# Performance work log

Measured on AMD Instinct MI355X. Metric: run time of the kernel, lower is better.

The kernel has to match this reference:

```python
import jax, jax.numpy as jnp
import numpy as np

G, N, F_IN, H, C = 128, 512, 128, 128, 10
LAMB = 1.0
NEG_SLOPE = 0.2
P_EDGE = 32.0 / N  # avg degree ~32


def setup_inputs() -> dict:
    key = jax.random.key(0)
    ks = jax.random.split(key, 12)
    x = jax.random.normal(ks[0], (G, N, F_IN), dtype=jnp.float32)
    # symmetric 0/1 adjacency without self loops (per-graph dense block)
    a = (jax.random.uniform(ks[1], (G, N, N)) < P_EDGE).astype(jnp.float32)
    adj = jnp.maximum(a, jnp.swapaxes(a, 1, 2)) * (1.0 - jnp.eye(N, dtype=jnp.float32))

    def lin(k, fi, fo):
        return (jax.random.normal(k, (fi, fo), dtype=jnp.float32) / np.float32(np.sqrt(fi)))

    return {
        "x": x, "adj": adj,
        "W1": lin(ks[2], F_IN, H), "b1": jnp.zeros((H,), jnp.float32),
        "W2": lin(ks[3], H, H), "b2": jnp.zeros((H,), jnp.float32),
        "W3": lin(ks[4], H, H), "b3": jnp.zeros((H,), jnp.float32),
        "att1_s": 0.1 * jax.random.normal(ks[5], (H,), dtype=jnp.float32),
        "att1_d": 0.1 * jax.random.normal(ks[6], (H,), dtype=jnp.float32),
        "att2_s": 0.1 * jax.random.normal(ks[7], (H,), dtype=jnp.float32),
        "att2_d": 0.1 * jax.random.normal(ks[8], (H,), dtype=jnp.float32),
        "Wl1": lin(ks[9], 2 * H, H), "bl1": jnp.zeros((H,), jnp.float32),
        "Wl2": lin(ks[10], H, H // 2), "bl2": jnp.zeros((H // 2,), jnp.float32),
        "Wl3": lin(ks[11], H // 2, C), "bl3": jnp.zeros((C,), jnp.float32),
    }


def gcn(x, adj, W, b):
    # GCNConv: D^{-1/2} (A + I) D^{-1/2} X W + b  (self-loop weight 1, edge weights in adj)
    deg = adj.sum(-1) + 1.0                              # [G, n]
    dinv = jax.lax.rsqrt(deg)
    xw = x @ W                                           # [G, n, H]
    agg = jnp.einsum('gij,gjf->gif', adj, dinv[..., None] * xw)
    return dinv[..., None] * agg + (dinv * dinv)[..., None] * xw + b


def info_score(x, adj):
    # HGP-SL node information score: row-wise L1 norm of (I - D^{-1} A) X
    deg = jnp.maximum(adj.sum(-1), 1.0)
    agg = jnp.einsum('gij,gjf->gif', adj, x) / deg[..., None]
    return jnp.sum(jnp.abs(x - agg), axis=-1)            # [G, n]


def hgpsl_pool(x, adj, att_s, att_d, k):
    # top-k node selection by information score, then structure learning:
    # dense (sample=False) path: e_ij = leaky_relu(att.[x_i||x_j]) + lamb*A_ij, softmax over j
    s = info_score(x, adj)
    _, idx = jax.lax.top_k(s, k)                         # [G, k]
    xk = jnp.take_along_axis(x, idx[..., None], axis=1)  # [G, k, H]
    g = jnp.arange(x.shape[0])[:, None, None]
    ak = adj[g, idx[:, :, None], idx[:, None, :]]        # induced adjacency [G, k, k]
    e = jax.nn.leaky_relu((xk @ att_s)[:, :, None] + (xk @ att_d)[:, None, :], NEG_SLOPE)
    attn = jax.nn.softmax(e + LAMB * ak, axis=-1)        # new learned edge weights
    return xk, attn


def readout(x):
    # gmp || gap over nodes
    return jnp.concatenate([x.max(axis=1), x.mean(axis=1)], axis=-1)


def reference(x, adj, W1, b1, W2, b2, W3, b3, att1_s, att1_d, att2_s, att2_d,
              Wl1, bl1, Wl2, bl2, Wl3, bl3):
    h = jax.nn.relu(gcn(x, adj, W1, b1))
    h, a1 = hgpsl_pool(h, adj, att1_s, att1_d, N // 2)
    x1 = readout(h)
    h = jax.nn.relu(gcn(h, a1, W2, b2))
    h, a2 = hgpsl_pool(h, a1, att2_s, att2_d, N // 4)
    x2 = readout(h)
    h = jax.nn.relu(gcn(h, a2, W3, b3))
    x3 = readout(h)
    z = jax.nn.relu(x1) + jax.nn.relu(x2) + jax.nn.relu(x3)
    z = jax.nn.relu(z @ Wl1 + bl1)
    z = jax.nn.relu(z @ Wl2 + bl2)
    return jax.nn.softmax(z @ Wl3 + bl3, axis=-1)
```

## Files before the change

kernel.cpp:

```cpp
#include <hip/hip_runtime.h>

#define Gg   128
#define N1   512
#define FH   128
#define K1   256
#define K2   128

typedef __bf16 bf16x8 __attribute__((ext_vector_type(8)));
typedef float  floatx4 __attribute__((ext_vector_type(4)));

__device__ inline float wredsum(float v) {
#pragma unroll
    for (int o = 32; o; o >>= 1) v += __shfl_xor(v, o, 64);
    return v;
}
__device__ inline float wredmax(float v) {
#pragma unroll
    for (int o = 32; o; o >>= 1) v = fmaxf(v, __shfl_xor(v, o, 64));
    return v;
}
__device__ inline unsigned short bf_rne(float x) {
    unsigned u = __float_as_uint(x);
    return (unsigned short)((u + 0x7fffu + ((u >> 16) & 1u)) >> 16);
}
__device__ __forceinline__ void gll16(const void* gsrc, void* lds) {
    __builtin_amdgcn_global_load_lds(
        (const __attribute__((address_space(1))) unsigned int*)gsrc,
        (__attribute__((address_space(3))) unsigned int*)lds, 16, 0, 0);
}

__global__ __launch_bounds__(256) void k_prep_gemm(const float* __restrict__ adj,
        unsigned short* __restrict__ adjbf,
        float* __restrict__ dinv_gcn, float* __restrict__ dinv_info,
        const float* __restrict__ A, const float* __restrict__ W, float* __restrict__ C) {
    __shared__ float Al[64][36];
    __shared__ float Wl[32][132];
    if (blockIdx.x < Gg * N1 / 64) {
        long long row0 = (long long)blockIdx.x * 64;
        int tid = threadIdx.x, tr = tid >> 4, tc = tid & 15;
        float acc[4][8] = {};
        for (int ch = 0; ch < 4; ++ch) {
            for (int p = tid; p < 512; p += 256) {
                int r = p >> 3, c4 = p & 7;
                *(float4*)&Al[r][c4 * 4] = *(const float4*)(A + (row0 + r) * 128 + ch * 32 + c4 * 4);
            }
            for (int p = tid; p < 1024; p += 256) {
                int r = p >> 5, c4 = p & 31;
                *(float4*)&Wl[r][c4 * 4] = *(const float4*)(W + (ch * 32 + r) * 128 + c4 * 4);
            }
            __syncthreads();
            for (int k = 0; k < 32; ++k) {
                float4 w0 = *(const float4*)&Wl[k][tc * 8];
                float4 w1 = *(const float4*)&Wl[k][tc * 8 + 4];
                float w[8] = {w0.x, w0.y, w0.z, w0.w, w1.x, w1.y, w1.z, w1.w};
#pragma unroll
                for (int i = 0; i < 4; ++i) {
                    float a = Al[tr * 4 + i][k];
#pragma unroll
                    for (int j = 0; j < 8; ++j) acc[i][j] = fmaf(a, w[j], acc[i][j]);
                }
            }
            __syncthreads();
        }
#pragma unroll
        for (int i = 0; i < 4; ++i) {
            long long r = row0 + tr * 4 + i;
            *(float4*)(C + r * 128 + tc * 8)     = make_float4(acc[i][0], acc[i][1], acc[i][2], acc[i][3]);
            *(float4*)(C + r * 128 + tc * 8 + 4) = make_float4(acc[i][4], acc[i][5], acc[i][6], acc[i][7]);
        }
    } else {
        int wave = threadIdx.x >> 6, lane = threadIdx.x & 63;
        long long row = (long long)(blockIdx.x - Gg * N1 / 64) * 4 + wave;
        const float* ar = adj + row * N1;
        float s = 0.f;
        unsigned short ub[8] __attribute__((aligned(16)));
#pragma unroll
        for (int c = 0; c < 2; ++c) {
            float4 v = *(const float4*)(ar + lane * 8 + c * 4);
            s += (v.x + v.y) + (v.z + v.w);
            ub[c * 4 + 0] = (unsigned short)(__float_as_uint(v.x) >> 16);
            ub[c * 4 + 1] = (unsigned short)(__float_as_uint(v.y) >> 16);
            ub[c * 4 + 2] = (unsigned short)(__float_as_uint(v.z) >> 16);
            ub[c * 4 + 3] = (unsigned short)(__float_as_uint(v.w) >> 16);
        }
        *(uint4*)(adjbf + row * N1 + lane * 8) = *(const uint4*)ub;
        s = wredsum(s);
        if (lane == 0) {
            dinv_gcn[row]  = rsqrtf(s + 1.0f);
            dinv_info[row] = 1.0f / fmaxf(s, 1.0f);
        }
    }
}

__global__ __launch_bounds__(256) void k_tsplit(const float* __restrict__ feat,
        const float* __restrict__ rs,
        unsigned short* __restrict__ Thi, unsigned short* __restrict__ Tmid,
        unsigned short* __restrict__ Tlo) {
    __shared__ float tile[64 * 65];
    int b = blockIdx.x;
    int g = b >> 4, rb = (b >> 1) & 7, cb = b & 1;
    int t = threadIdx.x;
    {
        int r0 = t >> 4, c4 = t & 15;
#pragma unroll
        for (int i = 0; i < 4; ++i) {
            int r = r0 + i * 16;
            float4 v = *(const float4*)(feat + ((long long)g * 512 + rb * 64 + r) * 128 + cb * 64 + c4 * 4);
            if (rs) {
                float sc = rs[(long long)g * 512 + rb * 64 + r];
                v.x *= sc; v.y *= sc; v.z *= sc; v.w *= sc;
            }
            tile[r * 65 + c4 * 4 + 0] = v.x;
            tile[r * 65 + c4 * 4 + 1] = v.y;
            tile[r * 65 + c4 * 4 + 2] = v.z;
            tile[r * 65 + c4 * 4 + 3] = v.w;
        }
    }
    __syncthreads();
    int tf = t >> 2, chunk = t & 3;
    unsigned short hbuf[16] __attribute__((aligned(16)));
    unsigned short mbuf[16] __attribute__((aligned(16)));
    unsigned short lbuf[16] __attribute__((aligned(16)));
#pragma unroll
    for (int i = 0; i < 16; ++i) {
        int m = chunk * 16 + i;
        float v = tile[m * 65 + tf];
        unsigned short h = bf_rne(v);
        float fh = __uint_as_float((unsigned)h << 16);
        float r1 = v - fh;
        unsigned short md = bf_rne(r1);
        float fm = __uint_as_float((unsigned)md << 16);
        float r2 = r1 - fm;
        unsigned short lo = bf_rne(r2);
        hbuf[i] = h; mbuf[i] = md; lbuf[i] = lo;
    }
    int sxz = (tf >> 1) & 3;
    int c0 = (chunk & 1) * 2;
    int p0 = (c0 ^ sxz) * 8, p1 = ((c0 + 1) ^ sxz) * 8;
    long long obase = (long long)g * 65536 + (rb * 2 + (chunk >> 1)) * 4096
                    + (cb * 64 + tf) * 32;
    *(uint4*)(Thi + obase + p0)  = *(const uint4*)&hbuf[0];
    *(uint4*)(Thi + obase + p1)  = *(const uint4*)&hbuf[8];
    *(uint4*)(Tmid + obase + p0) = *(const uint4*)&mbuf[0];
    *(uint4*)(Tmid + obase + p1) = *(const uint4*)&mbuf[8];
    *(uint4*)(Tlo + obase + p0)  = *(const uint4*)&lbuf[0];
    *(uint4*)(Tlo + obase + p1)  = *(const uint4*)&lbuf[8];
}

template<int EPI>
__global__ __launch_bounds__(256) void k_aggmm(const unsigned short* __restrict__ adjbf,
        const unsigned short* __restrict__ Bhi, const unsigned short* __restrict__ Bmid,
        const unsigned short* __restrict__ Blo,
        const float* __restrict__ dvec, const float* __restrict__ hx,
        const float* __restrict__ bias, float* __restrict__ outH, float* __restrict__ outS) {
    __shared__ unsigned short Al[2][4096];
    __shared__ unsigned short Blin[2][3][4096];
    __shared__ float sred[2][128];
    int b = blockIdx.x;
    int g  = (b & 7) + ((b >> 5) << 3);
    int rb = (b >> 3) & 3;
    int tid = threadIdx.x;
    int w = tid >> 6, lane = tid & 63;
    int wm = w >> 1, wn = w & 1;
    int ln = lane & 15, quad = lane >> 4;
    int aoff = ((quad ^ ((lane >> 1) & 3)) << 4);
    floatx4 acc[4][4];
#pragma unroll
    for (int i = 0; i < 4; ++i)
#pragma unroll
        for (int j = 0; j < 4; ++j) { floatx4 z = {0.f, 0.f, 0.f, 0.f}; acc[i][j] = z; }

    const char* bsrc0 = (const char*)(Bhi  + (long long)g * 65536);
    const char* bsrc1 = (const char*)(Bmid + (long long)g * 65536);
    const char* bsrc2 = (const char*)(Blo  + (long long)g * 65536);
    int r1 = w * 32 + (lane >> 2);
    int c1 = (lane & 3) ^ ((r1 >> 1) & 3);
    int r2 = r1 + 16;
    int c2 = (lane & 3) ^ ((r2 >> 1) & 3);
    const unsigned short* abase = adjbf + ((long long)g * 512 + rb * 128) * 512;
    const unsigned short* asrc1 = abase + (long long)r1 * 512 + c1 * 8;
    const unsigned short* asrc2 = abase + (long long)r2 * 512 + c2 * 8;

#define STAGE(bi, kkv) do {                                                   \
        char* aldst = (char*)&Al[bi][0] + w * 2048;                           \
        gll16(asrc1 + (kkv), aldst);                                          \
        gll16(asrc2 + (kkv), aldst + 1024);                                   \
        long long soff = (long long)((kkv) >> 5) * 8192 + (w * 2048) + (lane << 4); \
        char* l0 = (char*)&Blin[bi][0][0] + w * 2048;                         \
        char* l1 = (char*)&Blin[bi][1][0] + w * 2048;                         \
        char* l2 = (char*)&Blin[bi][2][0] + w * 2048;                         \
        gll16(bsrc0 + soff,        l0);                                       \
        gll16(bsrc0 + soff + 1024, l0 + 1024);                                \
        gll16(bsrc1 + soff,        l1);                                       \
        gll16(bsrc1 + soff + 1024, l1 + 1024);                                \
        gll16(bsrc2 + soff,        l2);                                       \
        gll16(bsrc2 + soff + 1024, l2 + 1024);                                \
    } while (0)

    STAGE(0, 0);
    for (int kk = 0; kk < 512; kk += 32) {
        int cur = (kk >> 5) & 1;
        if (kk + 32 < 512) {
            STAGE(cur ^ 1, kk + 32);
            asm volatile("s_waitcnt vmcnt(8)" ::: "memory");
        } else {
            asm volatile("s_waitcnt vmcnt(0)" ::: "memory");
        }
        __builtin_amdgcn_sched_barrier(0);
        __builtin_amdgcn_s_barrier();
        bf16x8 af[4];
#pragma unroll
        for (int tm = 0; tm < 4; ++tm)
            af[tm] = *(const bf16x8*)((const char*)&Al[cur][0] + (wm * 64 + tm * 16 + ln) * 64 + aoff);
#pragma unroll
        for (int s = 0; s < 3; ++s) {
#pragma unroll
            for (int tn = 0; tn < 4; ++tn) {
                bf16x8 bfr = *(const bf16x8*)((const char*)&Blin[cur][s][0]
                                              + (wn * 64 + tn * 16 + ln) * 64 + aoff);
#pragma unroll
                for (int tm = 0; tm < 4; ++tm)
                    acc[tm][tn] = __builtin_amdgcn_mfma_f32_16x16x32_bf16(af[tm], bfr, acc[tm][tn], 0, 0, 0);
            }
        }
        __builtin_amdgcn_sched_barrier(0);
        __builtin_amdgcn_s_barrier();
    }
#undef STAGE
    long long rowbase = (long long)g * 512 + rb * 128;
    if (EPI == 0) {
#pragma unroll
        for (int tm = 0; tm < 4; ++tm)
#pragma unroll
        for (int r = 0; r < 4; ++r) {
            int ml = wm * 64 + tm * 16 + quad * 4 + r;
            long long grow = rowbase + ml;
            float di = dvec[grow];
#pragma unroll
            for (int tn = 0; tn < 4; ++tn) {
                int nc = wn * 64 + tn * 16 + ln;
                float hv = hx[grow * 128 + nc];
                float o = fmaxf(fmaf(di, acc[tm][tn][r] + di * hv, bias[nc]), 0.f);
                outH[grow * 128 + nc] = o;
            }
        }
    } else {
#pragma unroll
        for (int tm = 0; tm < 4; ++tm)
#pragma unroll
        for (int r = 0; r < 4; ++r) {
            int ml = wm * 64 + tm * 16 + quad * 4 + r;
            long long grow = rowbase + ml;
            float di = dvec[grow];
            float v = 0.f;
#pragma unroll
            for (int tn = 0; tn < 4; ++tn) {
                int nc = wn * 64 + tn * 16 + ln;
                float hv = hx[grow * 128 + nc];
                v += fabsf(hv - acc[tm][tn][r] * di);
            }
            v += __shfl_xor(v, 1); v += __shfl_xor(v, 2);
            v += __shfl_xor(v, 4); v += __shfl_xor(v, 8);
            if (ln == 0) sred[wn][ml] = v;
        }
        __syncthreads();
        if (tid < 128) outS[rowbase + tid] = sred[0][tid] + sred[1][tid];
    }
}

__global__ __launch_bounds__(256) void k_gemm_rw(const float* __restrict__ A,
        const float* __restrict__ W, float* __restrict__ C,
        const float* __restrict__ rs) {
    __shared__ float Al[64][36];
    __shared__ float Wl[32][132];
    long long row0 = (long long)blockIdx.x * 64;
    int tid = threadIdx.x, tr = tid >> 4, tc = tid & 15;
    float acc[4][8] = {};
    for (int ch = 0; ch < 4; ++ch) {
        for (int p = tid; p < 512; p += 256) {
            int r = p >> 3, c4 = p & 7;
            *(float4*)&Al[r][c4 * 4] = *(const float4*)(A + (row0 + r) * 128 + ch * 32 + c4 * 4);
        }
        for (int p = tid; p < 1024; p += 256) {
            int r = p >> 5, c4 = p & 31;
            *(float4*)&Wl[r][c4 * 4] = *(const float4*)(W + (ch * 32 + r) * 128 + c4 * 4);
        }
        __syncthreads();
        for (int k = 0; k < 32; ++k) {
            float4 w0 = *(const float4*)&Wl[k][tc * 8];
            float4 w1 = *(const float4*)&Wl[k][tc * 8 + 4];
            float w[8] = {w0.x, w0.y, w0.z, w0.w, w1.x, w1.y, w1.z, w1.w};
#pragma unroll
            for (int i = 0; i < 4; ++i) {
                float a = Al[tr * 4 + i][k];
#pragma unroll
                for (int j = 0; j < 8; ++j) acc[i][j] = fmaf(a, w[j], acc[i][j]);
            }
        }
        __syncthreads();
    }
#pragma unroll
    for (int i = 0; i < 4; ++i) {
        long long r = row0 + tr * 4 + i;
        float sc = rs ? rs[r] : 1.0f;
        *(float4*)(C + r * 128 + tc * 8)     = make_float4(sc * acc[i][0], sc * acc[i][1], sc * acc[i][2], sc * acc[i][3]);
        *(float4*)(C + r * 128 + tc * 8 + 4) = make_float4(sc * acc[i][4], sc * acc[i][5], sc * acc[i][6], sc * acc[i][7]);
    }
}

template<int NT, int KSEL>
__global__ __launch_bounds__(256) void k_topk(const float* __restrict__ s, int* __restrict__ idx) {
    __shared__ unsigned long long keys[NT];
    int g = blockIdx.x;
    const float* sg = s + g * NT;
    for (int t = threadIdx.x; t < NT; t += 256) {
        unsigned int b = __float_as_uint(sg[t]);
        unsigned int ord = (b & 0x80000000u) ? ~b : (b | 0x80000000u);
        keys[t] = ((unsigned long long)(~ord) << 32) | (unsigned int)t;
    }
    __syncthreads();
    for (int k = 2; k <= NT; k <<= 1) {
        for (int j = k >> 1; j > 0; j >>= 1) {
            for (int i = threadIdx.x; i < NT; i += 256) {
                int l = i ^ j;
                if (l > i) {
                    bool dir = ((i & k) == 0);
                    unsigned long long a = keys[i], b2 = keys[l];
                    bool sw = dir ? (a > b2) : (a < b2);
                    if (sw) { keys[i] = b2; keys[l] = a; }
                }
            }
            __syncthreads();
        }
    }
    for (int t = threadIdx.x; t < KSEL; t += 256)
        idx[g * KSEL + t] = (int)(keys[t] & 0xffffffffu);
}

template<int KK>
__global__ __launch_bounds__(256) void k_gather(const float* __restrict__ h, int srcN,
        const int* __restrict__ idx, const float* __restrict__ atts, const float* __restrict__ attd,
        float* __restrict__ xk, float* __restrict__ as_, float* __restrict__ ad_) {
    int wave = threadIdx.x >> 6, lane = threadIdx.x & 63;
    int r = blockIdx.x * 4 + wave;
    int g = r / KK;
    int j = idx[r];
    float2 v = *(const float2*)(h + ((long long)g * srcN + j) * 128 + lane * 2);
    *(float2*)(xk + (long long)r * 128 + lane * 2) = v;
    float2 sv = *(const float2*)(atts + lane * 2);
    float2 dv = *(const float2*)(attd + lane * 2);
    float ps = v.x * sv.x + v.y * sv.y;
    float pd = v.x * dv.x + v.y * dv.y;
    ps = wredsum(ps); pd = wredsum(pd);
    if (lane == 0) { as_[r] = ps; ad_[r] = pd; }
}

template<int KK, int SRCN, bool BF16>
__global__ __launch_bounds__(256) void k_attnro(const void* __restrict__ adjSrc,
        const int* __restrict__ idx, const float* __restrict__ as_, const float* __restrict__ ad_,
        float* __restrict__ attn, float* __restrict__ dgo, float* __restrict__ dio,
        const float* __restrict__ xk, float* __restrict__ xo) {
    constexpr int E = KK / 64;
    constexpr int nAttn = Gg * KK / 4;
    __shared__ int   idxL[KK];
    __shared__ float adL[KK];
    __shared__ float rowL[4][SRCN];
    if ((int)blockIdx.x >= nAttn) {
        int g = blockIdx.x - nAttn, t = threadIdx.x;
        if (t < 128) {
            const float* p = xk + (long long)g * KK * 128 + t;
            float m = -1e30f, s = 0.f;
            for (int r = 0; r < KK; ++r) { float v = p[r * 128]; m = fmaxf(m, v); s += v; }
            xo[g * 256 + t] = m;
            xo[g * 256 + 128 + t] = s * (1.0f / KK);
        }
        return;
    }
    int bpg = KK / 4;
    int g = blockIdx.x / bpg;
    int wave = threadIdx.x >> 6, lane = threadIdx.x & 63;
    int i = (blockIdx.x % bpg) * 4 + wave;
    for (int t = threadIdx.x; t < KK; t += 256) { idxL[t] = idx[g * KK + t]; adL[t] = ad_[g * KK + t]; }
    __syncthreads();
    int ri = idxL[i];
    if (BF16) {
        const unsigned short* arow = (const unsigned short*)adjSrc + ((long long)g * SRCN + ri) * SRCN;
        for (int c = lane; c < SRCN; c += 64)
            rowL[wave][c] = __uint_as_float((unsigned)arow[c] << 16);
    } else {
        const float* arow = (const float*)adjSrc + ((long long)g * SRCN + ri) * SRCN;
        for (int c = lane; c < SRCN; c += 64) rowL[wave][c] = arow[c];
    }
    float asi = as_[g * KK + i];
    float vals[E];
    float m = -1e30f;
#pragma unroll
    for (int e = 0; e < E; ++e) {
        int j = e * 64 + lane;
        float x = asi + adL[j];
        x = (x >= 0.f) ? x : 0.2f * x;
        x += rowL[wave][idxL[j]];
        vals[e] = x; m = fmaxf(m, x);
    }
    m = wredmax(m);
    float S = 0.f;
#pragma unroll
    for (int e = 0; e < E; ++e) { vals[e] = expf(vals[e] - m); S += vals[e]; }
    S = wredsum(S);
    float inv = 1.f / S, rs = 0.f;
    float* orow = attn + ((long long)g * KK + i) * KK;
#pragma unroll
    for (int e = 0; e < E; ++e) { float p = vals[e] * inv; rs += p; orow[e * 64 + lane] = p; }
    rs = wredsum(rs);
    if (lane == 0) { dgo[g * KK + i] = rsqrtf(rs + 1.f); dio[g * KK + i] = 1.f / fmaxf(rs, 1.f); }
}

template<int KK, bool SCALEY, int EPI>
__global__ __launch_bounds__(256) void k_agg(const float* __restrict__ A, const float* __restrict__ Y,
        const float* __restrict__ dg, const float* __restrict__ di_,
        const float* __restrict__ bias, const float* __restrict__ hx,
        float* __restrict__ outH, float* __restrict__ outS) {
    __shared__ float Al[64][36];
    __shared__ float Yl[32][132];
    constexpr int RB = KK / 64;
    int g = blockIdx.x / RB;
    int rb = blockIdx.x % RB;
    const float* Ag = A + (long long)g * KK * KK;
    const float* Yg = Y + (long long)g * KK * 128;
    int tid = threadIdx.x, tr = tid >> 4, tc = tid & 15;
    float acc[4][8] = {};
    for (int ch = 0; ch < KK / 32; ++ch) {
        for (int p = tid; p < 512; p += 256) {
            int r = p >> 3, c4 = p & 7;
            *(float4*)&Al[r][c4 * 4] = *(const float4*)(Ag + (long long)(rb * 64 + r) * KK + ch * 32 + c4 * 4);
        }
        for (int p = tid; p < 1024; p += 256) {
            int r = p >> 5, c4 = p & 31;
            float4 v = *(const float4*)(Yg + (ch * 32 + r) * 128 + c4 * 4);
            if (SCALEY) { float sc = dg[g * KK + ch * 32 + r]; v.x *= sc; v.y *= sc; v.z *= sc; v.w *= sc; }
            *(float4*)&Yl[r][c4 * 4] = v;
        }
        __syncthreads();
        for (int k = 0; k < 32; ++k) {
            float4 w0 = *(const float4*)&Yl[k][tc * 8];
            float4 w1 = *(const float4*)&Yl[k][tc * 8 + 4];
            float w[8] = {w0.x, w0.y, w0.z, w0.w, w1.x, w1.y, w1.z, w1.w};
#pragma unroll
            for (int i = 0; i < 4; ++i) {
                float a = Al[tr * 4 + i][k];
#pragma unroll
                for (int j = 0; j < 8; ++j) acc[i][j] = fmaf(a, w[j], acc[i][j]);
            }
        }
        __syncthreads();
    }
    int i0 = rb * 64 + tr * 4;
    if (EPI == 0) {
#pragma unroll
        for (int i = 0; i < 4; ++i) {
            long long gi = (long long)g * KK + i0 + i;
            float d = dg[gi], dd = d * d;
            float4 x0 = *(const float4*)(hx + gi * 128 + tc * 8);
            float4 x1 = *(const float4*)(hx + gi * 128 + tc * 8 + 4);
            float4 b0 = *(const float4*)(bias + tc * 8);
            float4 b1 = *(const float4*)(bias + tc * 8 + 4);
            float4 o0, o1;
            o0.x = fmaxf(fmaf(d, acc[i][0], fmaf(dd, x0.x, b0.x)), 0.f);
            o0.y = fmaxf(fmaf(d, acc[i][1], fmaf(dd, x0.y, b0.y)), 0.f);
            o0.z = fmaxf(fmaf(d, acc[i][2], fmaf(dd, x0.z, b0.z)), 0.f);
            o0.w = fmaxf(fmaf(d, acc[i][3], fmaf(dd, x0.w, b0.w)), 0.f);
            o1.x = fmaxf(fmaf(d, acc[i][4], fmaf(dd, x1.x, b1.x)), 0.f);
            o1.y = fmaxf(fmaf(d, acc[i][5], fmaf(dd, x1.y, b1.y)), 0.f);
            o1.z = fmaxf(fmaf(d, acc[i][6], fmaf(dd, x1.z, b1.z)), 0.f);
            o1.w = fmaxf(fmaf(d, acc[i][7], fmaf(dd, x1.w, b1.w)), 0.f);
            *(float4*)(outH + gi * 128 + tc * 8)     = o0;
            *(float4*)(outH + gi * 128 + tc * 8 + 4) = o1;
        }
    } else {
        float* red = &Al[0][0];
#pragma unroll
        for (int i = 0; i < 4; ++i) {
            long long gi = (long long)g * KK + i0 + i;
            float d = di_[gi];
            float4 x0 = *(const float4*)(hx + gi * 128 + tc * 8);
            float4 x1 = *(const float4*)(hx + gi * 128 + tc * 8 + 4);
            float p = fabsf(x0.x - acc[i][0] * d) + fabsf(x0.y - acc[i][1] * d)
                    + fabsf(x0.z - acc[i][2] * d) + fabsf(x0.w - acc[i][3] * d)
                    + fabsf(x1.x - acc[i][4] * d) + fabsf(x1.y - acc[i][5] * d)
                    + fabsf(x1.z - acc[i][6] * d) + fabsf(x1.w - acc[i][7] * d);
            red[(tr * 4 + i) * 17 + tc] = p;
        }
        __syncthreads();
        if (tid < 64) {
            float s = 0.f;
#pragma unroll
            for (int t = 0; t < 16; ++t) s += red[tid * 17 + t];
            outS[(long long)g * KK + rb * 64 + tid] = s;
        }
    }
}

__global__ __launch_bounds__(128) void k_mlp(const float* __restrict__ x1, const float* __restrict__ x2,
        const float* __restrict__ h3,
        const float* __restrict__ Wl1, const float* __restrict__ bl1,
        const float* __restrict__ Wl2, const float* __restrict__ bl2,
        const float* __restrict__ Wl3, const float* __restrict__ bl3,
        float* __restrict__ out) {
    __shared__ float z[256], z1[128], z2[64], lg[10];
    int g = blockIdx.x, t = threadIdx.x;
    {
        const float* p = h3 + (long long)g * K2 * 128 + t;
        float m = -1e30f, s = 0.f;
        for (int r = 0; r < K2; ++r) { float v = p[r * 128]; m = fmaxf(m, v); s += v; }
        float x3a = m, x3b = s * (1.0f / K2);
        z[t]       = fmaxf(x1[g * 256 + t], 0.f)       + fmaxf(x2[g * 256 + t], 0.f)       + fmaxf(x3a, 0.f);
        z[t + 128] = fmaxf(x1[g * 256 + 128 + t], 0.f) + fmaxf(x2[g * 256 + 128 + t], 0.f) + fmaxf(x3b, 0.f);
    }
    __syncthreads();
    {
        float acc = bl1[t];
        for (int k = 0; k < 256; ++k) acc = fmaf(z[k], Wl1[k * 128 + t], acc);
        z1[t] = fmaxf(acc, 0.f);
    }
    __syncthreads();
    if (t < 64) {
        float acc = bl2[t];
        for (int k = 0; k < 128; ++k) acc = fmaf(z1[k], Wl2[k * 64 + t], acc);
        z2[t] = fmaxf(acc, 0.f);
    }
    __syncthreads();
    if (t < 10) {
        float acc = bl3[t];
        for (int k = 0; k < 64; ++k) acc = fmaf(z2[k], Wl3[k * 10 + t], acc);
        lg[t] = acc;
    }
    __syncthreads();
    if (t == 0) {
        float m = -1e30f;
        for (int c = 0; c < 10; ++c) m = fmaxf(m, lg[c]);
        float S = 0.f;
        float e[10];
        for (int c = 0; c < 10; ++c) { e[c] = expf(lg[c] - m); S += e[c]; }
        float inv = 1.f / S;
        for (int c = 0; c < 10; ++c) out[g * 10 + c] = e[c] * inv;
    }
}

extern "C" void kernel_launch(void* const* d_in, const int* in_sizes, int n_in,
                              void* d_out, int out_size, void* d_ws, size_t ws_size,
                              hipStream_t stream) {
    const float* x     = (const float*)d_in[0];
    const float* adj   = (const float*)d_in[1];
    const float* W1    = (const float*)d_in[2];
    const float* b1    = (const float*)d_in[3];
    const float* W2    = (const float*)d_in[4];
    const float* b2    = (const float*)d_in[5];
    const float* W3    = (const float*)d_in[6];
    const float* b3    = (const float*)d_in[7];
    const float* att1s = (const float*)d_in[8];
    const float* att1d = (const float*)d_in[9];
    const float* att2s = (const float*)d_in[10];
    const float* att2d = (const float*)d_in[11];
    const float* Wl1   = (const float*)d_in[12];
    const float* bl1   = (const float*)d_in[13];
    const float* Wl2   = (const float*)d_in[14];
    const float* bl2   = (const float*)d_in[15];
    const float* Wl3   = (const float*)d_in[16];
    const float* bl3   = (const float*)d_in[17];
    float* out = (float*)d_out;

    char* ws = (char*)d_ws;
    unsigned short* Thi  = (unsigned short*)(ws + 0);
    unsigned short* Tmid = (unsigned short*)(ws + 16777216);
    unsigned short* Tlo  = (unsigned short*)(ws + 33554432);
    float* xk1 = (float*)(ws + 0);
    float* xw2 = (float*)(ws + 16777216);
    float* h2  = (float*)(ws + 33554432);
    float* xk2 = (float*)(ws + 16777216);
    float* a2  = (float*)(ws + 25165824);
    float* xw3 = (float*)(ws + 0);
    float* h3  = (float*)(ws + 8388608);
    float* dxw1 = (float*)(ws + 50331648);
    float* h1   = dxw1;
    float* a1   = dxw1;
    float* s1      = (float*)(ws + 83886080);
    int*   idx1    = (int*)  (ws + 84148224);
    float* as1     = (float*)(ws + 84279296);
    float* ad1     = (float*)(ws + 84410368);
    float* dinv_g1 = (float*)(ws + 84541440);
    float* dinv_i1 = (float*)(ws + 84803584);
    float* dinv_g2 = (float*)(ws + 85065728);
    float* dinv_i2 = (float*)(ws + 85196800);
    float* x1r     = (float*)(ws + 85327872);
    float* s2      = (float*)(ws + 85458944);
    int*   idx2    = (int*)  (ws + 85590016);
    float* as2     = (float*)(ws + 85655552);
    float* ad2     = (float*)(ws + 85721088);
    float* dinv_g3 = (float*)(ws + 85786624);
    float* dinv_i3 = (float*)(ws + 85852160);
    float* x2r     = (float*)(ws + 85917696);
    unsigned short* adjbf = (unsigned short*)(ws + 100663296);

    k_prep_gemm<<<Gg * N1 / 64 + Gg * N1 / 4, 256, 0, stream>>>(adj, adjbf, dinv_g1, dinv_i1, x, W1, dxw1);
    k_tsplit<<<Gg * 16, 256, 0, stream>>>(dxw1, dinv_g1, Thi, Tmid, Tlo);
    k_aggmm<0><<<Gg * 4, 256, 0, stream>>>(adjbf, Thi, Tmid, Tlo, dinv_g1, dxw1, b1, h1, nullptr);
    k_tsplit<<<Gg * 16, 256, 0, stream>>>(h1, nullptr, Thi, Tmid, Tlo);
    k_aggmm<1><<<Gg * 4, 256, 0, stream>>>(adjbf, Thi, Tmid, Tlo, dinv_i1, h1, nullptr, nullptr, s1);
    k_topk<N1, K1><<<Gg, 256, 0, stream>>>(s1, idx1);
    k_gather<K1><<<Gg * K1 / 4, 256, 0, stream>>>(h1, N1, idx1, att1s, att1d, xk1, as1, ad1);
    k_attnro<K1, N1, true><<<Gg * K1 / 4 + Gg, 256, 0, stream>>>(adjbf, idx1, as1, ad1, a1, dinv_g2, dinv_i2, xk1, x1r);

    k_gemm_rw<<<Gg * K1 / 64, 256, 0, stream>>>(xk1, W2, xw2, nullptr);
    k_agg<K1, true, 0><<<Gg * (K1 / 64), 256, 0, stream>>>(a1, xw2, dinv_g2, dinv_i2, b2, xw2, h2, nullptr);
    k_agg<K1, false, 1><<<Gg * (K1 / 64), 256, 0, stream>>>(a1, h2, dinv_g2, dinv_i2, b2, h2, nullptr, s2);
    k_topk<K1, K2><<<Gg, 256, 0, stream>>>(s2, idx2);
    k_gather<K2><<<Gg * K2 / 4, 256, 0, stream>>>(h2, K1, idx2, att2s, att2d, xk2, as2, ad2);
    k_attnro<K2, K1, false><<<Gg * K2 / 4 + Gg, 256, 0, stream>>>(a1, idx2, as2, ad2, a2, dinv_g3, dinv_i3, xk2, x2r);

    k_gemm_rw<<<Gg * K2 / 64, 256, 0, stream>>>(xk2, W3, xw3, nullptr);
    k_agg<K2, true, 0><<<Gg * (K2 / 64), 256, 0, stream>>>(a2, xw3, dinv_g3, dinv_i3, b3, xw3, h3, nullptr);

    k_mlp<<<Gg, 128, 0, stream>>>(x1r, x2r, h3, Wl1, bl1, Wl2, bl2, Wl3, bl3, out);
}
```

Before: 606.2 us.

## Fold feature GEMM into attention kernel and widen k_agg reduction chunks

The standalone xk@W GEMM kernel is merged into the attention/readout kernel as extra blocks that share one shared-memory buffer, removing two kernel launches and letting the independent GEMM run alongside the attention work. Separately, the k_agg kernel now stages 64-wide K chunks instead of 32, halving the number of chunk iterations and barriers. The cost is more shared memory per block in both kernels, which may lower occupancy, especially in the merged kernel where every block reserves the larger buffer.

```diff
diff --git a/kernel.cpp b/kernel.cpp
--- a/kernel.cpp
+++ b/kernel.cpp
@@ -268,46 +268,6 @@
     }
 }
 
-__global__ __launch_bounds__(256) void k_gemm_rw(const float* __restrict__ A,
-        const float* __restrict__ W, float* __restrict__ C,
-        const float* __restrict__ rs) {
-    __shared__ float Al[64][36];
-    __shared__ float Wl[32][132];
-    long long row0 = (long long)blockIdx.x * 64;
-    int tid = threadIdx.x, tr = tid >> 4, tc = tid & 15;
-    float acc[4][8] = {};
-    for (int ch = 0; ch < 4; ++ch) {
-        for (int p = tid; p < 512; p += 256) {
-            int r = p >> 3, c4 = p & 7;
-            *(float4*)&Al[r][c4 * 4] = *(const float4*)(A + (row0 + r) * 128 + ch * 32 + c4 * 4);
-        }
-        for (int p = tid; p < 1024; p += 256) {
-            int r = p >> 5, c4 = p & 31;
-            *(float4*)&Wl[r][c4 * 4] = *(const float4*)(W + (ch * 32 + r) * 128 + c4 * 4);
-        }
-        __syncthreads();
-        for (int k = 0; k < 32; ++k) {
-            float4 w0 = *(const float4*)&Wl[k][tc * 8];
-            float4 w1 = *(const float4*)&Wl[k][tc * 8 + 4];
-            float w[8] = {w0.x, w0.y, w0.z, w0.w, w1.x, w1.y, w1.z, w1.w};
-#pragma unroll
-            for (int i = 0; i < 4; ++i) {
-                float a = Al[tr * 4 + i][k];
-#pragma unroll
-                for (int j = 0; j < 8; ++j) acc[i][j] = fmaf(a, w[j], acc[i][j]);
-            }
-        }
-        __syncthreads();
-    }
-#pragma unroll
-    for (int i = 0; i < 4; ++i) {
-        long long r = row0 + tr * 4 + i;
-        float sc = rs ? rs[r] : 1.0f;
-        *(float4*)(C + r * 128 + tc * 8)     = make_float4(sc * acc[i][0], sc * acc[i][1], sc * acc[i][2], sc * acc[i][3]);
-        *(float4*)(C + r * 128 + tc * 8 + 4) = make_float4(sc * acc[i][4], sc * acc[i][5], sc * acc[i][6], sc * acc[i][7]);
-    }
-}
-
 template<int NT, int KSEL>
 __global__ __launch_bounds__(256) void k_topk(const float* __restrict__ s, int* __restrict__ idx) {
     __shared__ unsigned long long keys[NT];
@@ -356,17 +316,55 @@
 }
 
 template<int KK, int SRCN, bool BF16>
-__global__ __launch_bounds__(256) void k_attnro(const void* __restrict__ adjSrc,
+__global__ __launch_bounds__(256) void k_attnro_gemm(const void* __restrict__ adjSrc,
         const int* __restrict__ idx, const float* __restrict__ as_, const float* __restrict__ ad_,
         float* __restrict__ attn, float* __restrict__ dgo, float* __restrict__ dio,
-        const float* __restrict__ xk, float* __restrict__ xo) {
+        const float* __restrict__ xk, float* __restrict__ xo,
+        const float* __restrict__ W, float* __restrict__ xwout) {
     constexpr int E = KK / 64;
     constexpr int nAttn = Gg * KK / 4;
-    __shared__ int   idxL[KK];
-    __shared__ float adL[KK];
-    __shared__ float rowL[4][SRCN];
-    if ((int)blockIdx.x >= nAttn) {
-        int g = blockIdx.x - nAttn, t = threadIdx.x;
+    constexpr int nGemmBase = nAttn + Gg;
+    __shared__ float smem[6528];
+    int b = blockIdx.x;
+    if (b >= nGemmBase) {
+        float (*Al)[36]  = (float(*)[36])&smem[0];
+        float (*Wl)[132] = (float(*)[132])&smem[2304];
+        long long row0 = (long long)(b - nGemmBase) * 64;
+        int tid = threadIdx.x, tr = tid >> 4, tc = tid & 15;
+        float acc[4][8] = {};
+        for (int ch = 0; ch < 4; ++ch) {
+            for (int p = tid; p < 512; p += 256) {
+                int r = p >> 3, c4 = p & 7;
+                *(float4*)&Al[r][c4 * 4] = *(const float4*)(xk + (row0 + r) * 128 + ch * 32 + c4 * 4);
+            }
+            for (int p = tid; p < 1024; p += 256) {
+                int r = p >> 5, c4 = p & 31;
+                *(float4*)&Wl[r][c4 * 4] = *(const float4*)(W + (ch * 32 + r) * 128 + c4 * 4);
+            }
+            __syncthreads();
+            for (int k = 0; k < 32; ++k) {
+                float4 w0 = *(const float4*)&Wl[k][tc * 8];
+                float4 w1 = *(const float4*)&Wl[k][tc * 8 + 4];
+                float w[8] = {w0.x, w0.y, w0.z, w0.w, w1.x, w1.y, w1.z, w1.w};
+#pragma unroll
+                for (int i = 0; i < 4; ++i) {
+                    float a = Al[tr * 4 + i][k];
+#pragma unroll
+                    for (int j = 0; j < 8; ++j) acc[i][j] = fmaf(a, w[j], acc[i][j]);
+                }
+            }
+            __syncthreads();
+        }
+#pragma unroll
+        for (int i = 0; i < 4; ++i) {
+            long long r = row0 + tr * 4 + i;
+            *(float4*)(xwout + r * 128 + tc * 8)     = make_float4(acc[i][0], acc[i][1], acc[i][2], acc[i][3]);
+            *(float4*)(xwout + r * 128 + tc * 8 + 4) = make_float4(acc[i][4], acc[i][5], acc[i][6], acc[i][7]);
+        }
+        return;
+    }
+    if (b >= nAttn) {
+        int g = b - nAttn, t = threadIdx.x;
         if (t < 128) {
             const float* p = xk + (long long)g * KK * 128 + t;
             float m = -1e30f, s = 0.f;
@@ -376,20 +374,23 @@
         }
         return;
     }
+    int* idxL   = (int*)&smem[0];
+    float* adL  = &smem[KK];
+    float* rowL = &smem[2 * KK];
     int bpg = KK / 4;
-    int g = blockIdx.x / bpg;
+    int g = b / bpg;
     int wave = threadIdx.x >> 6, lane = threadIdx.x & 63;
-    int i = (blockIdx.x % bpg) * 4 + wave;
+    int i = (b % bpg) * 4 + wave;
     for (int t = threadIdx.x; t < KK; t += 256) { idxL[t] = idx[g * KK + t]; adL[t] = ad_[g * KK + t]; }
     __syncthreads();
     int ri = idxL[i];
     if (BF16) {
         const unsigned short* arow = (const unsigned short*)adjSrc + ((long long)g * SRCN + ri) * SRCN;
         for (int c = lane; c < SRCN; c += 64)
-            rowL[wave][c] = __uint_as_float((unsigned)arow[c] << 16);
+            rowL[wave * SRCN + c] = __uint_as_float((unsigned)arow[c] << 16);
     } else {
         const float* arow = (const float*)adjSrc + ((long long)g * SRCN + ri) * SRCN;
-        for (int c = lane; c < SRCN; c += 64) rowL[wave][c] = arow[c];
+        for (int c = lane; c < SRCN; c += 64) rowL[wave * SRCN + c] = arow[c];
     }
     float asi = as_[g * KK + i];
     float vals[E];
@@ -399,7 +400,7 @@
         int j = e * 64 + lane;
         float x = asi + adL[j];
         x = (x >= 0.f) ? x : 0.2f * x;
-        x += rowL[wave][idxL[j]];
+        x += rowL[wave * SRCN + idxL[j]];
         vals[e] = x; m = fmaxf(m, x);
     }
     m = wredmax(m);
@@ -420,8 +421,9 @@
         const float* __restrict__ dg, const float* __restrict__ di_,
         const float* __restrict__ bias, const float* __restrict__ hx,
         float* __restrict__ outH, float* __restrict__ outS) {
-    __shared__ float Al[64][36];
-    __shared__ float Yl[32][132];
+    __shared__ float Al[64][68];
+    __shared__ float Yl[64][132];
+    __shared__ float red[64][17];
     constexpr int RB = KK / 64;
     int g = blockIdx.x / RB;
     int rb = blockIdx.x % RB;
@@ -429,19 +431,19 @@
     const float* Yg = Y + (long long)g * KK * 128;
     int tid = threadIdx.x, tr = tid >> 4, tc = tid & 15;
     float acc[4][8] = {};
-    for (int ch = 0; ch < KK / 32; ++ch) {
-        for (int p = tid; p < 512; p += 256) {
-            int r = p >> 3, c4 = p & 7;
-            *(float4*)&Al[r][c4 * 4] = *(const float4*)(Ag + (long long)(rb * 64 + r) * KK + ch * 32 + c4 * 4);
-        }
+    for (int ch = 0; ch < KK / 64; ++ch) {
         for (int p = tid; p < 1024; p += 256) {
+            int r = p >> 4, c4 = p & 15;
+            *(float4*)&Al[r][c4 * 4] = *(const float4*)(Ag + (rb * 64 + r) * KK + ch * 64 + c4 * 4);
+        }
+        for (int p = tid; p < 2048; p += 256) {
             int r = p >> 5, c4 = p & 31;
-            float4 v = *(const float4*)(Yg + (ch * 32 + r) * 128 + c4 * 4);
-            if (SCALEY) { float sc = dg[g * KK + ch * 32 + r]; v.x *= sc; v.y *= sc; v.z *= sc; v.w *= sc; }
+            float4 v = *(const float4*)(Yg + (ch * 64 + r) * 128 + c4 * 4);
+            if (SCALEY) { float sc = dg[g * KK + ch * 64 + r]; v.x *= sc; v.y *= sc; v.z *= sc; v.w *= sc; }
             *(float4*)&Yl[r][c4 * 4] = v;
         }
         __syncthreads();
-        for (int k = 0; k < 32; ++k) {
+        for (int k = 0; k < 64; ++k) {
             float4 w0 = *(const float4*)&Yl[k][tc * 8];
             float4 w1 = *(const float4*)&Yl[k][tc * 8 + 4];
             float w[8] = {w0.x, w0.y, w0.z, w0.w, w1.x, w1.y, w1.z, w1.w};
@@ -477,7 +479,6 @@
             *(float4*)(outH + gi * 128 + tc * 8 + 4) = o1;
         }
     } else {
-        float* red = &Al[0][0];
 #pragma unroll
         for (int i = 0; i < 4; ++i) {
             long long gi = (long long)g * KK + i0 + i;
@@ -488,13 +489,13 @@
                     + fabsf(x0.z - acc[i][2] * d) + fabsf(x0.w - acc[i][3] * d)
                     + fabsf(x1.x - acc[i][4] * d) + fabsf(x1.y - acc[i][5] * d)
                     + fabsf(x1.z - acc[i][6] * d) + fabsf(x1.w - acc[i][7] * d);
-            red[(tr * 4 + i) * 17 + tc] = p;
+            red[tr * 4 + i][tc] = p;
         }
         __syncthreads();
         if (tid < 64) {
             float s = 0.f;
 #pragma unroll
-            for (int t = 0; t < 16; ++t) s += red[tid * 17 + t];
+            for (int t = 0; t < 16; ++t) s += red[tid][t];
             outS[(long long)g * KK + rb * 64 + tid] = s;
         }
     }
@@ -608,16 +609,16 @@
     k_aggmm<1><<<Gg * 4, 256, 0, stream>>>(adjbf, Thi, Tmid, Tlo, dinv_i1, h1, nullptr, nullptr, s1);
     k_topk<N1, K1><<<Gg, 256, 0, stream>>>(s1, idx1);
     k_gather<K1><<<Gg * K1 / 4, 256, 0, stream>>>(h1, N1, idx1, att1s, att1d, xk1, as1, ad1);
-    k_attnro<K1, N1, true><<<Gg * K1 / 4 + Gg, 256, 0, stream>>>(adjbf, idx1, as1, ad1, a1, dinv_g2, dinv_i2, xk1, x1r);
-
-    k_gemm_rw<<<Gg * K1 / 64, 256, 0, stream>>>(xk1, W2, xw2, nullptr);
+    k_attnro_gemm<K1, N1, true><<<Gg * K1 / 4 + Gg + Gg * K1 / 64, 256, 0, stream>>>(
+        adjbf, idx1, as1, ad1, a1, dinv_g2, dinv_i2, xk1, x1r, W2, xw2);
+
     k_agg<K1, true, 0><<<Gg * (K1 / 64), 256, 0, stream>>>(a1, xw2, dinv_g2, dinv_i2, b2, xw2, h2, nullptr);
     k_agg<K1, false, 1><<<Gg * (K1 / 64), 256, 0, stream>>>(a1, h2, dinv_g2, dinv_i2, b2, h2, nullptr, s2);
     k_topk<K1, K2><<<Gg, 256, 0, stream>>>(s2, idx2);
     k_gather<K2><<<Gg * K2 / 4, 256, 0, stream>>>(h2, K1, idx2, att2s, att2d, xk2, as2, ad2);
-    k_attnro<K2, K1, false><<<Gg * K2 / 4 + Gg, 256, 0, stream>>>(a1, idx2, as2, ad2, a2, dinv_g3, dinv_i3, xk2, x2r);
-
-    k_gemm_rw<<<Gg * K2 / 64, 256, 0, stream>>>(xk2, W3, xw3, nullptr);
+    k_attnro_gemm<K2, K1, false><<<Gg * K2 / 4 + Gg + Gg * K2 / 64, 256, 0, stream>>>(
+        a1, idx2, as2, ad2, a2, dinv_g3, dinv_i3, xk2, x2r, W3, xw3);
+
     k_agg<K2, true, 0><<<Gg * (K2 / 64), 256, 0, stream>>>(a2, xw3, dinv_g3, dinv_i3, b3, xw3, h3, nullptr);
 
     k_mlp<<<Gg, 128, 0, stream>>>(x1r, x2r, h3, Wl1, bl1, Wl2, bl2, Wl3, bl3, out);
```

New measurement: 595.5 us. About the same (-1.8%).
